# Performance work log

Measured on AMD Instinct MI355X. Metric: run time of the kernel, lower is better.

Reference implementation:

```python
import jax, jax.numpy as jnp
import numpy as np

CODEBOOK_SIZE = 1024
EMBEDDING_DIM = 256
COMMITMENT_COST = 0.25


def setup_inputs() -> dict:
    key = jax.random.key(0)
    k1, k2 = jax.random.split(key)
    x = jax.random.normal(k1, (32, EMBEDDING_DIM, 32, 32), dtype=jnp.float32)
    # embedding initialized uniform(-1/K, 1/K) like the torch module
    embedding = jax.random.uniform(
        k2, (CODEBOOK_SIZE, EMBEDDING_DIM), dtype=jnp.float32,
        minval=-1.0 / CODEBOOK_SIZE, maxval=1.0 / CODEBOOK_SIZE)
    return {"x": x, "embedding": embedding}


def reference(x, embedding):
    # x: [B, C, H, W] -> inputs: [B, H, W, C]
    inputs = jnp.transpose(x, (0, 2, 3, 1))
    input_shape = inputs.shape
    flat = inputs.reshape(-1, EMBEDDING_DIM)  # [N, D]
    # squared L2 distances to codebook: [N, K]
    distances = (jnp.sum(flat ** 2, axis=1, keepdims=True)
                 + jnp.sum(embedding ** 2, axis=1)
                 - 2.0 * flat @ embedding.T)
    encoding_indices = jnp.argmin(distances, axis=1)  # [N]
    encodings = jax.nn.one_hot(encoding_indices, CODEBOOK_SIZE, dtype=jnp.float32)  # [N, K]
    # gather (same math as encodings @ embedding)
    quantized = embedding[encoding_indices].reshape(input_shape)  # [B, H, W, C]
    e_latent_loss = jnp.mean((jax.lax.stop_gradient(quantized) - inputs) ** 2)
    q_latent_loss = jnp.mean((quantized - jax.lax.stop_gradient(inputs)) ** 2)
    loss = q_latent_loss + COMMITMENT_COST * e_latent_loss
    # straight-through estimator
    quantized_st = inputs + jax.lax.stop_gradient(quantized - inputs)
    return (loss, jnp.transpose(quantized_st, (0, 3, 1, 2)), encodings)
```

## Files before the change

kernel.cpp:

```cpp
#include <hip/hip_runtime.h>
#include <cstdint>
#include <cstddef>

constexpr int B = 32, C = 256, H = 32, W = 32;
constexpr int NPTS = B * H * W;
constexpr int DIM  = 256;
constexpr int K    = 1024;
constexpr int QELEMS = B * C * H * W;
constexpr int CHW = C * H * W;

typedef __attribute__((ext_vector_type(8))) short s8v;
typedef __attribute__((ext_vector_type(4))) float f32x4;

#define GLD_LDS16(g, l)                                                        \
  __builtin_amdgcn_global_load_lds(                                            \
      (const __attribute__((address_space(1))) unsigned int*)(g),              \
      (__attribute__((address_space(3))) unsigned int*)(l), 16, 0, 0)

__device__ __forceinline__ unsigned short f2bf(float f) {
  unsigned u = __float_as_uint(f);
  return (unsigned short)((u + 0x7FFFu + ((u >> 16) & 1u)) >> 16);
}

__global__ __launch_bounds__(256) void prep_kernel(
    const float* __restrict__ x, const float* __restrict__ emb,
    unsigned short* __restrict__ ehi, float* __restrict__ esq,
    unsigned short* __restrict__ xhi, float* __restrict__ xsq,
    float* __restrict__ loss) {
  __shared__ float xls[DIM][64];
  const int t = threadIdx.x;

  if (blockIdx.x < 16) {
    if (blockIdx.x == 0 && t == 0) *loss = 0.f;
    float (*sums)[64] = (float (*)[64])xls;
    const int k = blockIdx.x * 64 + (t & 63);
    const int seg = t >> 6;
    const float* er = emb + (size_t)k * DIM + seg * 64;
    float v[64];
    float4* v4 = (float4*)v;
#pragma unroll
    for (int i = 0; i < 16; ++i) v4[i] = *(const float4*)(er + i * 4);
    float s = 0.f;
#pragma unroll
    for (int i = 0; i < 64; ++i) s = fmaf(v[i], v[i], s);
    unsigned short* eo = ehi + (size_t)k * DIM + seg * 64;
#pragma unroll
    for (int i = 0; i < 8; ++i) {
      unsigned short h[8];
#pragma unroll
      for (int j = 0; j < 8; ++j) h[j] = f2bf(v[i * 8 + j]);
      *(s8v*)(eo + i * 8) = *(s8v*)h;
    }
    sums[seg][t & 63] = s;
    __syncthreads();
    if (t < 64)
      esq[blockIdx.x * 64 + t] =
          ((sums[0][t] + sums[1][t]) + sums[2][t]) + sums[3][t];
    return;
  }

  const int n0 = (blockIdx.x - 16) * 64;
  const int bb = n0 >> 10, hw0 = n0 & 1023;
  const int p = t & 63, cs = t >> 6;
  const float* xb = x + (size_t)bb * CHW + hw0;
#pragma unroll 8
  for (int r = 0; r < 64; ++r) {
    const int c = r * 4 + cs;
    xls[c][p] = xb[(size_t)c * 1024 + p];
  }
  __syncthreads();
  if (t < 64) {
    float s = 0.f;
#pragma unroll 8
    for (int c = 0; c < 256; ++c) {
      const float v = xls[c][t];
      s = fmaf(v, v, s);
    }
    xsq[n0 + t] = s;
  }
  const int p2 = t >> 2, cb = (t & 3) * 64;
  unsigned short* xo = xhi + (size_t)(n0 + p2) * DIM + cb;
#pragma unroll
  for (int i = 0; i < 8; ++i) {
    unsigned short h[8];
#pragma unroll
    for (int j = 0; j < 8; ++j) h[j] = f2bf(xls[cb + i * 8 + j][p2]);
    *(s8v*)(xo + i * 8) = *(s8v*)h;
  }
}

constexpr float MARGIN = 1e-3f;
__global__ __launch_bounds__(256) void coarse_kernel(
    const unsigned short* __restrict__ xhi, const unsigned short* __restrict__ ehi,
    const float* __restrict__ esq, const float* __restrict__ xsq,
    float* __restrict__ part, unsigned int* __restrict__ cand,
    float* __restrict__ encz) {
  __shared__ __align__(16) unsigned short xs[128][32];
  __shared__ __align__(16) unsigned short es[128][32];
  __shared__ float xsq_s[128], esq_s[128], thr_s[128];
  __shared__ unsigned long long red2[2][128];
  __shared__ unsigned int cntL[128];

  const int t = threadIdx.x;
  const int lane = t & 63, w = t >> 6;
  const int wn = (w & 1) * 64, wk = (w >> 1) * 64;
  const int col = lane & 15, quad = lane >> 4;
  const int nblk = blockIdx.x * 128;
  const int kblk = blockIdx.y * 128;

  if (t < 128) {
    xsq_s[t] = xsq[nblk + t];
    esq_s[t] = esq[kblk + t];
    cntL[t] = 0u;
  }

  f32x4 acc[4][4];
#pragma unroll
  for (int i = 0; i < 4; ++i)
#pragma unroll
    for (int j = 0; j < 4; ++j) acc[i][j] = (f32x4){0.f, 0.f, 0.f, 0.f};

  const int gl_row = lane >> 2;
  const int gl_c   = (lane & 3) * 8;

  for (int c0 = 0; c0 < DIM; c0 += 32) {
    __syncthreads();
#pragma unroll
    for (int i = 0; i < 2; ++i) {
      const int inst = w + 4 * i;
      const int row = inst * 16 + gl_row;
      GLD_LDS16(xhi + (size_t)(nblk + row) * DIM + c0 + gl_c, &xs[inst * 16][0]);
      GLD_LDS16(ehi + (size_t)(kblk + row) * DIM + c0 + gl_c, &es[inst * 16][0]);
    }
    __syncthreads();
    s8v a[4], b[4];
#pragma unroll
    for (int ti = 0; ti < 4; ++ti)
      a[ti] = *(const s8v*)&xs[wn + ti * 16 + col][quad * 8];
#pragma unroll
    for (int tj = 0; tj < 4; ++tj)
      b[tj] = *(const s8v*)&es[wk + tj * 16 + col][quad * 8];
#pragma unroll
    for (int ti = 0; ti < 4; ++ti)
#pragma unroll
      for (int tj = 0; tj < 4; ++tj)
        acc[ti][tj] = __builtin_amdgcn_mfma_f32_16x16x32_bf16(
            a[ti], b[tj], acc[ti][tj], 0, 0, 0);
  }

  {
    const size_t bidx = (size_t)blockIdx.y * gridDim.x + blockIdx.x;
    float* sl = encz + bidx * 16384;
    float4* b4 = (float4*)(sl + 3);
    const float4 z4 = {0.f, 0.f, 0.f, 0.f};
#pragma unroll
    for (int j = 0; j < 16; ++j) {
      const int idx = t + j * 256;
      if (idx < 4095) b4[idx] = z4;
    }
    if (t == 0) { sl[0] = 0.f; sl[1] = 0.f; sl[2] = 0.f; sl[16383] = 0.f; }
  }

  unsigned long long nmin[4][4];
#pragma unroll
  for (int ti = 0; ti < 4; ++ti)
#pragma unroll
    for (int r = 0; r < 4; ++r) nmin[ti][r] = ~0ULL;
#pragma unroll
  for (int ti = 0; ti < 4; ++ti)
#pragma unroll
    for (int tj = 0; tj < 4; ++tj) {
      const int krel = wk + tj * 16 + col;
      const float eq = esq_s[krel];
#pragma unroll
      for (int r = 0; r < 4; ++r) {
        const int nl = wn + ti * 16 + quad * 4 + r;
        const float d = (xsq_s[nl] + eq) - 2.f * acc[ti][tj][r];
        const unsigned long long key =
            ((unsigned long long)__float_as_uint(d) << 32) |
            (unsigned)(kblk + krel);
        if (key < nmin[ti][r]) nmin[ti][r] = key;
      }
    }
#pragma unroll
  for (int o = 1; o < 16; o <<= 1)
#pragma unroll
    for (int ti = 0; ti < 4; ++ti)
#pragma unroll
      for (int r = 0; r < 4; ++r) {
        const unsigned long long v = __shfl_xor(nmin[ti][r], o, 64);
        if (v < nmin[ti][r]) nmin[ti][r] = v;
      }
  if (col == 0) {
#pragma unroll
    for (int ti = 0; ti < 4; ++ti)
#pragma unroll
      for (int r = 0; r < 4; ++r)
        red2[w >> 1][wn + ti * 16 + quad * 4 + r] = nmin[ti][r];
  }
  __syncthreads();
  if (t < 128) {
    const unsigned long long m0 = red2[0][t], m1 = red2[1][t];
    const unsigned long long m = (m1 < m0) ? m1 : m0;
    const float dmin = __uint_as_float((unsigned)(m >> 32));
    part[(size_t)(nblk + t) * 8 + blockIdx.y] = dmin;
    thr_s[t] = dmin + MARGIN;
  }
  __syncthreads();
#pragma unroll
  for (int ti = 0; ti < 4; ++ti)
#pragma unroll
    for (int tj = 0; tj < 4; ++tj) {
      const int krel = wk + tj * 16 + col;
      const float eq = esq_s[krel];
#pragma unroll
      for (int r = 0; r < 4; ++r) {
        const int nl = wn + ti * 16 + quad * 4 + r;
        const float d = (xsq_s[nl] + eq) - 2.f * acc[ti][tj][r];
        if (d <= thr_s[nl]) {
          const unsigned slot = atomicAdd(&cntL[nl], 1u);
          if (slot < 4u)
            cand[((size_t)(nblk + nl) * 8 + blockIdx.y) * 4 + slot] =
                (unsigned)(kblk + krel);
        }
      }
    }
  __syncthreads();
  if (t < 128) {
    unsigned c = cntL[t];
    const size_t base = ((size_t)(nblk + t) * 8 + blockIdx.y) * 4;
    if (c > 4u) { cand[base + 3] = 0xFFFFFFFEu; c = 3u; }
    for (unsigned s = c; s < 4u; ++s) cand[base + s] = 0xFFFFFFFFu;
  }
}

__global__ __launch_bounds__(256) void finish_kernel(
    const float* __restrict__ x, const float* __restrict__ emb,
    const float* __restrict__ esq, const float* __restrict__ xsq,
    const float* __restrict__ part, const unsigned int* __restrict__ cand,
    float* __restrict__ outq, float* __restrict__ enc,
    float* __restrict__ loss) {
  __shared__ __align__(16) float xls[DIM][17];
  __shared__ unsigned list[512];
  __shared__ unsigned long long best[16];
  __shared__ float thr_s[16];
  __shared__ float xsq_s[16];
  __shared__ float lred[4];
  __shared__ int ids[16];
  __shared__ int lcnt;

  const int t = threadIdx.x;
  const int n0 = blockIdx.x * 16;
  const int bb = n0 >> 10, hw0 = n0 & 1023;

  const float* xb = x + (size_t)bb * CHW + hw0;
  {
    const int p = t & 15, cs = t >> 4;
#pragma unroll 4
    for (int r = 0; r < 16; ++r) {
      const int c = r * 16 + cs;
      xls[c][p] = xb[(size_t)c * 1024 + p];
    }
  }
  if (t == 0) lcnt = 0;
  if (t < 16) {
    best[t] = ~0ULL;
    xsq_s[t] = xsq[n0 + t];
    const float4 p0 = *(const float4*)&part[(size_t)(n0 + t) * 8];
    const float4 p1 = *(const float4*)&part[(size_t)(n0 + t) * 8 + 4];
    float g = fminf(fminf(fminf(p0.x, p0.y), fminf(p0.z, p0.w)),
                    fminf(fminf(p1.x, p1.y), fminf(p1.z, p1.w)));
    thr_s[t] = g + MARGIN;
  }
  __syncthreads();

  if (t < 128) {
    const int nn = t >> 3, s = t & 7;
    const float pv = part[(size_t)(n0 + nn) * 8 + s];
    if (pv <= thr_s[nn]) {
      const uint4 c4 = *(const uint4*)&cand[((size_t)(n0 + nn) * 8 + s) * 4];
      const unsigned vs[4] = {c4.x, c4.y, c4.z, c4.w};
#pragma unroll
      for (int i = 0; i < 4; ++i) {
        const unsigned v = vs[i];
        if (v == 0xFFFFFFFFu) continue;
        const unsigned entry = (v == 0xFFFFFFFEu)
                                   ? ((unsigned)nn << 11) | 1024u | (unsigned)s
                                   : ((unsigned)nn << 11) | (v & 1023u);
        const int pos = atomicAdd(&lcnt, 1);
        if (pos < 512) list[pos] = entry;
      }
    }
  }
  __syncthreads();

  const int L = lcnt < 512 ? lcnt : 512;
  for (int e = t; e < L; e += 256) {
    const unsigned entry = list[e];
    const int p = entry >> 11;
    const float xq = xsq_s[p];
    int klo, khi;
    if (entry & 1024u) { const int s = entry & 7; klo = s * 128; khi = klo + 128; }
    else               { klo = entry & 1023u; khi = klo + 1; }
    for (int k = klo; k < khi; ++k) {
      const float* er = emb + (size_t)k * DIM;
      float dot = 0.f;
#pragma unroll 4
      for (int c4 = 0; c4 < DIM; c4 += 4) {
        const float4 e4 = *(const float4*)(er + c4);
        dot = fmaf(xls[c4 + 0][p], e4.x, dot);
        dot = fmaf(xls[c4 + 1][p], e4.y, dot);
        dot = fmaf(xls[c4 + 2][p], e4.z, dot);
        dot = fmaf(xls[c4 + 3][p], e4.w, dot);
      }
      const float t1 = xq + esq[k];
      const float d = t1 - 2.f * dot;
      const unsigned long long key =
          ((unsigned long long)__float_as_uint(d) << 32) | (unsigned)k;
      atomicMin(&best[p], key);
    }
  }
  __syncthreads();
  if (t < 16) ids[t] = (int)(best[t] & 0xFFFFFFFFu);
  __syncthreads();

  float lsum = 0.f;
  {
    const int p = t & 15, g = t >> 4;
    const int row = ids[p];
    const float* er = emb + (size_t)row * DIM + g * 16;
    float* ob = outq + (size_t)bb * CHW + hw0 + p;
#pragma unroll
    for (int i = 0; i < 4; ++i) {
      const float4 v = *(const float4*)(er + i * 4);
      const int c = g * 16 + i * 4;
      float d0 = v.x - xls[c + 0][p];
      float d1 = v.y - xls[c + 1][p];
      float d2 = v.z - xls[c + 2][p];
      float d3 = v.w - xls[c + 3][p];
      ob[(size_t)(c + 0) * 1024] = v.x;
      ob[(size_t)(c + 1) * 1024] = v.y;
      ob[(size_t)(c + 2) * 1024] = v.z;
      ob[(size_t)(c + 3) * 1024] = v.w;
      lsum = fmaf(d0, d0, lsum);
      lsum = fmaf(d1, d1, lsum);
      lsum = fmaf(d2, d2, lsum);
      lsum = fmaf(d3, d3, lsum);
    }
  }

  if (t < 16) enc[(size_t)(n0 + t) * K + ids[t]] = 1.0f;

  float s = lsum;
#pragma unroll
  for (int o = 32; o > 0; o >>= 1) s += __shfl_down(s, o, 64);
  if ((t & 63) == 0) lred[t >> 6] = s;
  __syncthreads();
  if (t == 0) {
    const float tot = (((lred[0] + lred[1]) + lred[2]) + lred[3]) *
                      (1.25f / (float)QELEMS);
    atomicAdd(loss, tot);
  }
}

extern "C" void kernel_launch(void* const* d_in, const int* in_sizes, int n_in,
                              void* d_out, int out_size, void* d_ws, size_t ws_size,
                              hipStream_t stream) {
  const float* x   = (const float*)d_in[0];
  const float* emb = (const float*)d_in[1];
  float* out  = (float*)d_out;
  float* loss = out;
  float* outq = out + 1;
  float* enc  = out + 1 + QELEMS;

  char* ws = (char*)d_ws;
  unsigned short* ehi  = (unsigned short*)ws;
  float*          esq  = (float*)(ws + 524288);
  float*          xsq  = (float*)(ws + 528384);
  float*          part = (float*)(ws + 659456);
  unsigned int*   cand = (unsigned int*)(ws + 1708032);
  unsigned short* xhi  = (unsigned short*)(ws + 5902336);

  prep_kernel<<<16 + NPTS / 64, 256, 0, stream>>>(x, emb, ehi, esq, xhi, xsq,
                                                  loss);
  dim3 cg(NPTS / 128, 8);
  coarse_kernel<<<cg, 256, 0, stream>>>(xhi, ehi, esq, xsq, part, cand, enc);
  finish_kernel<<<NPTS / 16, 256, 0, stream>>>(x, emb, esq, xsq, part, cand,
                                               outq, enc, loss);
}
```

Baseline: 287.8 us.

## Move one-hot zeroing into prep kernel and replace loss atomics with reduction

The zero-fill of the one-hot encodings output moves out of the coarse GEMM kernel into extra blocks of the prep kernel, which is memory-bound anyway. The prep kernel also loads x with direct global-to-LDS transfers over 32-point tiles instead of 64. The per-block atomicAdd on the loss becomes a write to a workspace array, summed by a new single-block reduction kernel, which gives a deterministic order. This costs one more launch and makes the prep kernel heavier.

```diff
diff --git a/kernel.cpp b/kernel.cpp
--- a/kernel.cpp
+++ b/kernel.cpp
@@ -26,14 +26,14 @@
     const float* __restrict__ x, const float* __restrict__ emb,
     unsigned short* __restrict__ ehi, float* __restrict__ esq,
     unsigned short* __restrict__ xhi, float* __restrict__ xsq,
-    float* __restrict__ loss) {
-  __shared__ float xls[DIM][64];
+    float* __restrict__ encz) {
+  __shared__ float xls[DIM][32];
   const int t = threadIdx.x;
-
-  if (blockIdx.x < 16) {
-    if (blockIdx.x == 0 && t == 0) *loss = 0.f;
+  const int bid = blockIdx.x;
+
+  if (bid < 16) {
     float (*sums)[64] = (float (*)[64])xls;
-    const int k = blockIdx.x * 64 + (t & 63);
+    const int k = bid * 64 + (t & 63);
     const int seg = t >> 6;
     const float* er = emb + (size_t)k * DIM + seg * 64;
     float v[64];
@@ -54,22 +54,42 @@
     sums[seg][t & 63] = s;
     __syncthreads();
     if (t < 64)
-      esq[blockIdx.x * 64 + t] =
+      esq[bid * 64 + t] =
           ((sums[0][t] + sums[1][t]) + sums[2][t]) + sums[3][t];
     return;
   }
 
-  const int n0 = (blockIdx.x - 16) * 64;
+  const int u = bid - 16;
+  const int g = u / 3, r = u - g * 3;
+
+  if (r != 0) {
+    const size_t bidx = (size_t)g * 2 + (r - 1);
+    float* sl = encz + bidx * 16384;
+    float4* b4 = (float4*)(sl + 3);
+    const float4 z4 = {0.f, 0.f, 0.f, 0.f};
+#pragma unroll
+    for (int j = 0; j < 16; ++j) {
+      const int idx = t + j * 256;
+      if (idx < 4095) b4[idx] = z4;
+    }
+    if (t == 0) { sl[0] = 0.f; sl[1] = 0.f; sl[2] = 0.f; sl[16383] = 0.f; }
+    return;
+  }
+
+  const int n0 = g * 32;
   const int bb = n0 >> 10, hw0 = n0 & 1023;
-  const int p = t & 63, cs = t >> 6;
   const float* xb = x + (size_t)bb * CHW + hw0;
-#pragma unroll 8
-  for (int r = 0; r < 64; ++r) {
-    const int c = r * 4 + cs;
-    xls[c][p] = xb[(size_t)c * 1024 + p];
-  }
-  __syncthreads();
-  if (t < 64) {
+  const int lane = t & 63, w = t >> 6;
+  const int row_off = lane >> 3;
+  const int p4 = (lane & 7) * 4;
+#pragma unroll
+  for (int i = 0; i < 8; ++i) {
+    const int c0 = w * 64 + i * 8;
+    GLD_LDS16(xb + (size_t)(c0 + row_off) * 1024 + p4, &xls[c0][0]);
+  }
+  __syncthreads();
+
+  if (t < 32) {
     float s = 0.f;
 #pragma unroll 8
     for (int c = 0; c < 256; ++c) {
@@ -78,10 +98,10 @@
     }
     xsq[n0 + t] = s;
   }
-  const int p2 = t >> 2, cb = (t & 3) * 64;
+  const int p2 = t & 31, cb = (t >> 5) * 32;
   unsigned short* xo = xhi + (size_t)(n0 + p2) * DIM + cb;
 #pragma unroll
-  for (int i = 0; i < 8; ++i) {
+  for (int i = 0; i < 4; ++i) {
     unsigned short h[8];
 #pragma unroll
     for (int j = 0; j < 8; ++j) h[j] = f2bf(xls[cb + i * 8 + j][p2]);
@@ -93,8 +113,7 @@
 __global__ __launch_bounds__(256) void coarse_kernel(
     const unsigned short* __restrict__ xhi, const unsigned short* __restrict__ ehi,
     const float* __restrict__ esq, const float* __restrict__ xsq,
-    float* __restrict__ part, unsigned int* __restrict__ cand,
-    float* __restrict__ encz) {
+    float* __restrict__ part, unsigned int* __restrict__ cand) {
   __shared__ __align__(16) unsigned short xs[128][32];
   __shared__ __align__(16) unsigned short es[128][32];
   __shared__ float xsq_s[128], esq_s[128], thr_s[128];
@@ -146,19 +165,6 @@
       for (int tj = 0; tj < 4; ++tj)
         acc[ti][tj] = __builtin_amdgcn_mfma_f32_16x16x32_bf16(
             a[ti], b[tj], acc[ti][tj], 0, 0, 0);
-  }
-
-  {
-    const size_t bidx = (size_t)blockIdx.y * gridDim.x + blockIdx.x;
-    float* sl = encz + bidx * 16384;
-    float4* b4 = (float4*)(sl + 3);
-    const float4 z4 = {0.f, 0.f, 0.f, 0.f};
-#pragma unroll
-    for (int j = 0; j < 16; ++j) {
-      const int idx = t + j * 256;
-      if (idx < 4095) b4[idx] = z4;
-    }
-    if (t == 0) { sl[0] = 0.f; sl[1] = 0.f; sl[2] = 0.f; sl[16383] = 0.f; }
   }
 
   unsigned long long nmin[4][4];
@@ -239,7 +245,7 @@
     const float* __restrict__ esq, const float* __restrict__ xsq,
     const float* __restrict__ part, const unsigned int* __restrict__ cand,
     float* __restrict__ outq, float* __restrict__ enc,
-    float* __restrict__ loss) {
+    float* __restrict__ lws) {
   __shared__ __align__(16) float xls[DIM][17];
   __shared__ unsigned list[512];
   __shared__ unsigned long long best[16];
@@ -356,11 +362,23 @@
   for (int o = 32; o > 0; o >>= 1) s += __shfl_down(s, o, 64);
   if ((t & 63) == 0) lred[t >> 6] = s;
   __syncthreads();
-  if (t == 0) {
-    const float tot = (((lred[0] + lred[1]) + lred[2]) + lred[3]) *
-                      (1.25f / (float)QELEMS);
-    atomicAdd(loss, tot);
-  }
+  if (t == 0)
+    lws[blockIdx.x] = ((lred[0] + lred[1]) + lred[2]) + lred[3];
+}
+
+__global__ __launch_bounds__(256) void loss_reduce(
+    const float* __restrict__ lws, float* __restrict__ loss) {
+  __shared__ float red[4];
+  const int t = threadIdx.x;
+  float s = 0.f;
+#pragma unroll
+  for (int i = 0; i < 8; ++i) s += lws[t + i * 256];
+#pragma unroll
+  for (int o = 32; o > 0; o >>= 1) s += __shfl_down(s, o, 64);
+  if ((t & 63) == 0) red[t >> 6] = s;
+  __syncthreads();
+  if (t == 0)
+    *loss = (((red[0] + red[1]) + red[2]) + red[3]) * (1.25f / (float)QELEMS);
 }
 
 extern "C" void kernel_launch(void* const* d_in, const int* in_sizes, int n_in,
@@ -380,11 +398,12 @@
   float*          part = (float*)(ws + 659456);
   unsigned int*   cand = (unsigned int*)(ws + 1708032);
   unsigned short* xhi  = (unsigned short*)(ws + 5902336);
-
-  prep_kernel<<<16 + NPTS / 64, 256, 0, stream>>>(x, emb, ehi, esq, xhi, xsq,
-                                                  loss);
+  float*          lws  = (float*)(ws + 22679552);
+
+  prep_kernel<<<16 + 3072, 256, 0, stream>>>(x, emb, ehi, esq, xhi, xsq, enc);
   dim3 cg(NPTS / 128, 8);
-  coarse_kernel<<<cg, 256, 0, stream>>>(xhi, ehi, esq, xsq, part, cand, enc);
+  coarse_kernel<<<cg, 256, 0, stream>>>(xhi, ehi, esq, xsq, part, cand);
   finish_kernel<<<NPTS / 16, 256, 0, stream>>>(x, emb, esq, xsq, part, cand,
-                                               outq, enc, loss);
-}
+                                               outq, enc, lws);
+  loss_reduce<<<1, 256, 0, stream>>>(lws, loss);
+}
```

New measurement: 290.6 us. No clear change (+1.0%).
